# Kernel optimization log

Measured on AMD Instinct MI355X. Metric: run time of the kernel, lower is better.

Reference implementation:

```python
import jax, jax.numpy as jnp
import numpy as np

C = 32
KSHAPE = (C, C, 3, 3)  # (C_out, C_in, kH, kW)
BN_EPS = 1e-5


def _binary_act(x):
    # forward: sign(x); backward: identity clipped to |x|<1 (STE)
    xc = jnp.clip(x, -1.0, 1.0)
    return jax.lax.stop_gradient(jnp.sign(x) - xc) + xc


def _binarize_weight(w_flat, shape):
    w = w_flat.reshape(shape)
    scale = jax.lax.stop_gradient(jnp.mean(jnp.abs(w)))  # global scalar scale, detached
    wc = jnp.clip(w, -1.0, 1.0)
    # forward: scale*sign(w); backward flows through clamp(w,-1,1)
    return jax.lax.stop_gradient(scale * jnp.sign(w) - wc) + wc


def _bi_conv_bn(x, w_flat, gamma, beta, stride):
    xb = _binary_act(x)
    w = _binarize_weight(w_flat, KSHAPE)
    y = jax.lax.conv_general_dilated(
        xb, w, window_strides=(stride, stride), padding=[(1, 1), (1, 1)],
        dimension_numbers=('NCHW', 'OIHW', 'NCHW'))
    # BatchNorm2d in training mode (batch stats, biased variance)
    m = jnp.mean(y, axis=(0, 2, 3), keepdims=True)
    v = jnp.mean((y - m) ** 2, axis=(0, 2, 3), keepdims=True)
    yhat = (y - m) * jax.lax.rsqrt(v + BN_EPS)
    return gamma.reshape(1, -1, 1, 1) * yhat + beta.reshape(1, -1, 1, 1)


def setup_inputs() -> dict:
    key = jax.random.key(0)
    k1, k2, k3 = jax.random.split(key, 3)
    return {
        'x': jax.random.normal(k1, (32, C, 160, 160), dtype=jnp.float32),
        'w1': jax.random.normal(k2, (C * C * 9, 1), dtype=jnp.float32) * 0.05,
        'gamma1': jnp.ones((C,), dtype=jnp.float32),
        'beta1': jnp.zeros((C,), dtype=jnp.float32),
        'w2': jax.random.normal(k3, (C * C * 9, 1), dtype=jnp.float32) * 0.05,
        'gamma2': jnp.ones((C,), dtype=jnp.float32),
        'beta2': jnp.zeros((C,), dtype=jnp.float32),
    }


def reference(x, w1, gamma1, beta1, w2, gamma2, beta2):
    # bireal residual block, stride=1 => skip_op is Identity
    inner = _bi_conv_bn(x, w1, gamma1, beta1, 1) + x
    out = _bi_conv_bn(inner, w2, gamma2, beta2, 1) + inner
    return out
```

## Files before the change

kernel.cpp:

```cpp
#include <hip/hip_runtime.h>
#include <stdint.h>

#define NIMG 32
#define CH 32
#define HH 160
#define WW 160
#define HWL (HH*WW)
#define PRS 164
#define PHH 162
#define PIMG (PHH*PRS)
#define NPIX (NIMG*HWL)
#define HALO_WORDS 968

#define OFF_P     0
#define OFF_P2    3400704
#define OFF_INNER (OFF_P2 + 3400704)
#define OFF_WP    (OFF_INNER + 52428800)
#define OFF_CORR  (OFF_WP + 2304)
#define OFF_SC    (OFF_CORR + 2304)
#define OFF_SB    (OFF_SC + 128)

struct StatLine {
  int s1; int pad0; unsigned long long s2; char pad[112];
};

#define AS1 __attribute__((address_space(1)))
#define AS3 __attribute__((address_space(3)))
__device__ __forceinline__ void dma16(const void* g, void* l) {
  __builtin_amdgcn_global_load_lds((const AS1 void*)g, (AS3 void*)l, 16, 0, 0);
}

__device__ __forceinline__ unsigned short f2bf(float f) {
  unsigned u = __float_as_uint(f);
  u += 0x7fffu + ((u >> 16) & 1u);
  return (unsigned short)(u >> 16);
}
__device__ __forceinline__ float bf2f(unsigned short u) {
  return __uint_as_float((uint32_t)u << 16);
}

__device__ __forceinline__ void conv4(const uint32_t r[3][6], const uint32_t* wsh,
                                      int co, int& a0, int& a1, int& a2, int& a3)
{
  a0 = a1 = a2 = a3 = 0;
  #pragma unroll
  for (int dy = 0; dy < 3; ++dy) {
    #pragma unroll
    for (int dx = 0; dx < 3; ++dx) {
      uint32_t wvv = wsh[co * 9 + dy * 3 + dx];
      a0 += __popc(r[dy][0 + dx] ^ wvv);
      a1 += __popc(r[dy][1 + dx] ^ wvv);
      a2 += __popc(r[dy][2 + dx] ^ wvv);
      a3 += __popc(r[dy][3 + dx] ^ wvv);
    }
  }
}

__global__ __launch_bounds__(256) void pack_prep(const float* __restrict__ x,
    const float* __restrict__ w1, const float* __restrict__ w2,
    uint32_t* __restrict__ P, uint32_t* __restrict__ P2, uint32_t* __restrict__ WP,
    int* __restrict__ CORR, float* __restrict__ SC, StatLine* __restrict__ SB)
{
  __shared__ float lds[8192];
  const int tid = threadIdx.x;
  const int b = blockIdx.x;

  if (b >= 3200) {
    if (b == 3442) {
      int* z = (int*)SB;
      for (int i = tid; i < 2048; i += 256) z[i] = 0;
      float* red = lds;
      uint32_t* wpl = (uint32_t*)(lds + 256);
      for (int cv = 0; cv < 2; ++cv) {
        const float* w = cv ? w2 : w1;
        float s = 0.f;
        #pragma unroll
        for (int j = 0; j < 9; ++j) {
          float4 v = *reinterpret_cast<const float4*>(w + (j * 256 + tid) * 4);
          s += fabsf(v.x) + fabsf(v.y) + fabsf(v.z) + fabsf(v.w);
        }
        red[tid] = s;
        __syncthreads();
        for (int st = 128; st > 0; st >>= 1) {
          if (tid < st) red[tid] += red[tid + st];
          __syncthreads();
        }
        if (tid == 0) SC[cv] = red[0] / 9216.0f;
        for (int i = tid; i < 288; i += 256) {
          int co = i / 9, t = i - co * 9;
          uint32_t bw = 0;
          for (int ci = 0; ci < 32; ++ci)
            bw |= (w[(co * 32 + ci) * 9 + t] > 0.0f) ? (1u << ci) : 0u;
          WP[cv * 288 + i] = bw;
          wpl[i] = bw;
        }
        __syncthreads();
        for (int i = tid; i < 288; i += 256) {
          int cls = i / 32, co = i - cls * 32;
          int hc = cls / 3, wc = cls - hc * 3;
          int corr = 0;
          for (int t = 0; t < 9; ++t) {
            int dy = t / 3 - 1, dx = t % 3 - 1;
            bool inval = (hc == 0 && dy == -1) || (hc == 2 && dy == 1) ||
                         (wc == 0 && dx == -1) || (wc == 2 && dx == 1);
            if (inval) corr += 32 - 2 * __popc(wpl[co * 9 + t]);
          }
          CORR[cv * 288 + cls * 32 + co] = corr;
        }
        __syncthreads();
      }
    } else {
      int k = (b - 3200) * 256 + tid;
      uint32_t* buf = (k < 32 * HALO_WORDS) ? P : P2;
      int j = k % (32 * HALO_WORDS);
      int img = j / HALO_WORDS;
      int r = j - img * HALO_WORDS;
      int pr, pc;
      if (r < 164)      { pr = 0;   pc = r; }
      else if (r < 328) { pr = 161; pc = r - 164; }
      else {
        int k2 = r - 328;
        pr = 1 + (k2 >> 2);
        int q = k2 & 3;
        pc = (q == 0) ? 0 : (160 + q);
      }
      buf[img * PIMG + pr * PRS + pc] = 0;
    }
    return;
  }

  int n = b / 100;
  int p0 = (b - n * 100) * 256;
  const float* xb = x + (size_t)n * CH * HWL + p0;
  #pragma unroll
  for (int it = 0; it < 8; ++it) {
    int c = it * 4 + (tid >> 6);
    const float* g = xb + (size_t)c * HWL + (tid & 63) * 4;
    dma16(g, lds + c * 256);
  }
  __syncthreads();

  uint32_t bits = 0;
  #pragma unroll
  for (int c = 0; c < 32; ++c) {
    if (lds[c * 256 + tid] > 0.f) bits |= 1u << c;
  }
  int px = p0 + tid;
  int h = px / WW, w = px - h * WW;
  P[n * PIMG + (h + 1) * PRS + (w + 1)] = bits;
}

__global__ __launch_bounds__(256) void conv_stats(const uint32_t* __restrict__ P,
    const uint32_t* __restrict__ WP, const int* __restrict__ CORR,
    StatLine* __restrict__ sb)
{
  __shared__ uint32_t wsh[288];
  __shared__ int csh[288];
  __shared__ int ls1[32], ls2[32];
  const int tid = threadIdx.x;
  for (int i = tid; i < 288; i += 256) { wsh[i] = WP[i]; csh[i] = CORR[i]; }
  if (tid < 32) { ls1[tid] = 0; ls2[tid] = 0; }
  __syncthreads();

  int g = blockIdx.x * 256 + tid;
  int w4 = g % 40;
  int t1 = g / 40;
  int h = t1 % 160;
  int n = t1 / 160;

  const uint32_t* base = P + n * PIMG + h * PRS + w4 * 4;
  uint32_t r[3][6];
  #pragma unroll
  for (int dy = 0; dy < 3; ++dy) {
    uint4 a = *reinterpret_cast<const uint4*>(base + dy * PRS);
    uint2 bw = *reinterpret_cast<const uint2*>(base + dy * PRS + 4);
    r[dy][0] = a.x; r[dy][1] = a.y; r[dy][2] = a.z; r[dy][3] = a.w;
    r[dy][4] = bw.x; r[dy][5] = bw.y;
  }

  int rowc = (h == 0) ? 0 : ((h == 159) ? 6 : 3);
  int cls0  = rowc + ((w4 == 0) ? 0 : 1);
  int cls12 = rowc + 1;
  int cls3  = rowc + ((w4 == 39) ? 2 : 1);
  int lane = tid & 63;

  #pragma unroll
  for (int co = 0; co < 32; ++co) {
    int a0, a1, a2, a3;
    conv4(r, wsh, co, a0, a1, a2, a3);
    int d0 = 288 - 2 * a0 - csh[cls0 * 32 + co];
    int d1 = 288 - 2 * a1 - csh[cls12 * 32 + co];
    int d2 = 288 - 2 * a2 - csh[cls12 * 32 + co];
    int d3 = 288 - 2 * a3 - csh[cls3 * 32 + co];
    int ds = d0 + d1 + d2 + d3;
    int sq = d0 * d0 + d1 * d1 + d2 * d2 + d3 * d3;
    #pragma unroll
    for (int off = 32; off > 0; off >>= 1) {
      ds += __shfl_down(ds, off);
      sq += __shfl_down(sq, off);
    }
    if (lane == 0) { atomicAdd(&ls1[co], ds); atomicAdd(&ls2[co], sq); }
  }
  __syncthreads();
  if (tid < 32) {
    atomicAdd(&sb[tid].s1, ls1[tid]);
    atomicAdd(&sb[tid].s2, (unsigned long long)(long long)ls2[tid]);
  }
}

__global__ __launch_bounds__(256, 2) void conv_bn1(const uint32_t* __restrict__ P,
    const uint32_t* __restrict__ WP, const int* __restrict__ CORR,
    const float* __restrict__ x, const float* __restrict__ SCp,
    const StatLine* __restrict__ sb, const float* __restrict__ gamma,
    const float* __restrict__ beta, unsigned short* __restrict__ INNER,
    uint32_t* __restrict__ P2)
{
  __shared__ uint32_t wsh[288];
  __shared__ int csh[288];
  __shared__ float Ash[32], Bsh[32];
  const int tid = threadIdx.x;
  for (int i = tid; i < 288; i += 256) { wsh[i] = WP[i]; csh[i] = CORR[i]; }
  if (tid < 32) {
    double sc = (double)SCp[0];
    double m  = sc * (double)sb[tid].s1 / (double)NPIX;
    double ms = sc * sc * (double)(long long)sb[tid].s2 / (double)NPIX;
    float inv = (float)(1.0 / sqrt(ms - m * m + 1e-5));
    float gm = gamma[tid];
    Ash[tid] = gm * inv * (float)sc;
    Bsh[tid] = beta[tid] - gm * inv * (float)m;
  }
  __syncthreads();

  int g = blockIdx.x * 256 + tid;
  int w4 = g % 40;
  int t1 = g / 40;
  int h = t1 % 160;
  int n = t1 / 160;

  const uint32_t* base = P + n * PIMG + h * PRS + w4 * 4;
  uint32_t r[3][6];
  #pragma unroll
  for (int dy = 0; dy < 3; ++dy) {
    uint4 a = *reinterpret_cast<const uint4*>(base + dy * PRS);
    uint2 bw = *reinterpret_cast<const uint2*>(base + dy * PRS + 4);
    r[dy][0] = a.x; r[dy][1] = a.y; r[dy][2] = a.z; r[dy][3] = a.w;
    r[dy][4] = bw.x; r[dy][5] = bw.y;
  }
  int rowc = (h == 0) ? 0 : ((h == 159) ? 6 : 3);
  int cls0  = rowc + ((w4 == 0) ? 0 : 1);
  int cls12 = rowc + 1;
  int cls3  = rowc + ((w4 == 39) ? 2 : 1);

  int i = h * WW + w4 * 4;
  size_t pbase = (size_t)n * CH * HWL + i;

  float4 xv[32];
  #pragma unroll
  for (int j = 0; j < 32; ++j)
    xv[j] = *reinterpret_cast<const float4*>(x + pbase + (size_t)j * HWL);

  uint32_t bb0 = 0, bb1 = 0, bb2 = 0, bb3 = 0;
  #pragma unroll
  for (int co = 0; co < 32; ++co) {
    int a0, a1, a2, a3;
    conv4(r, wsh, co, a0, a1, a2, a3);
    int d0 = 288 - 2 * a0 - csh[cls0 * 32 + co];
    int d1 = 288 - 2 * a1 - csh[cls12 * 32 + co];
    int d2 = 288 - 2 * a2 - csh[cls12 * 32 + co];
    int d3 = 288 - 2 * a3 - csh[cls3 * 32 + co];
    float A = Ash[co], Bv = Bsh[co];
    float v0 = fmaf(A, (float)d0, Bv) + xv[co].x;
    float v1 = fmaf(A, (float)d1, Bv) + xv[co].y;
    float v2 = fmaf(A, (float)d2, Bv) + xv[co].z;
    float v3 = fmaf(A, (float)d3, Bv) + xv[co].w;
    ushort4 o; o.x = f2bf(v0); o.y = f2bf(v1); o.z = f2bf(v2); o.w = f2bf(v3);
    *reinterpret_cast<ushort4*>(INNER + pbase + (size_t)co * HWL) = o;
    uint32_t m = 1u << co;
    if (v0 > 0.f) bb0 |= m;
    if (v1 > 0.f) bb1 |= m;
    if (v2 > 0.f) bb2 |= m;
    if (v3 > 0.f) bb3 |= m;
  }
  uint32_t* pw = P2 + n * PIMG + (h + 1) * PRS + (w4 * 4 + 1);
  pw[0] = bb0; pw[1] = bb1; pw[2] = bb2; pw[3] = bb3;
}

__global__ __launch_bounds__(256, 2) void conv_bn2(const uint32_t* __restrict__ P2,
    const uint32_t* __restrict__ WP, const int* __restrict__ CORR,
    const unsigned short* __restrict__ INNER, const float* __restrict__ SCp,
    const StatLine* __restrict__ sb, const float* __restrict__ gamma,
    const float* __restrict__ beta, float* __restrict__ out)
{
  __shared__ uint32_t wsh[288];
  __shared__ int csh[288];
  __shared__ float Ash[32], Bsh[32];
  const int tid = threadIdx.x;
  for (int i = tid; i < 288; i += 256) { wsh[i] = WP[i]; csh[i] = CORR[i]; }
  if (tid < 32) {
    double sc = (double)SCp[0];
    double m  = sc * (double)sb[tid].s1 / (double)NPIX;
    double ms = sc * sc * (double)(long long)sb[tid].s2 / (double)NPIX;
    float inv = (float)(1.0 / sqrt(ms - m * m + 1e-5));
    float gm = gamma[tid];
    Ash[tid] = gm * inv * (float)sc;
    Bsh[tid] = beta[tid] - gm * inv * (float)m;
  }
  __syncthreads();

  int g = blockIdx.x * 256 + tid;
  int w4 = g % 40;
  int t1 = g / 40;
  int h = t1 % 160;
  int n = t1 / 160;

  const uint32_t* base = P2 + n * PIMG + h * PRS + w4 * 4;
  uint32_t r[3][6];
  #pragma unroll
  for (int dy = 0; dy < 3; ++dy) {
    uint4 a = *reinterpret_cast<const uint4*>(base + dy * PRS);
    uint2 bw = *reinterpret_cast<const uint2*>(base + dy * PRS + 4);
    r[dy][0] = a.x; r[dy][1] = a.y; r[dy][2] = a.z; r[dy][3] = a.w;
    r[dy][4] = bw.x; r[dy][5] = bw.y;
  }
  int rowc = (h == 0) ? 0 : ((h == 159) ? 6 : 3);
  int cls0  = rowc + ((w4 == 0) ? 0 : 1);
  int cls12 = rowc + 1;
  int cls3  = rowc + ((w4 == 39) ? 2 : 1);

  int i = h * WW + w4 * 4;
  size_t pbase = (size_t)n * CH * HWL + i;

  ushort4 iv[32];
  #pragma unroll
  for (int j = 0; j < 32; ++j)
    iv[j] = *reinterpret_cast<const ushort4*>(INNER + pbase + (size_t)j * HWL);

  #pragma unroll
  for (int co = 0; co < 32; ++co) {
    int a0, a1, a2, a3;
    conv4(r, wsh, co, a0, a1, a2, a3);
    int d0 = 288 - 2 * a0 - csh[cls0 * 32 + co];
    int d1 = 288 - 2 * a1 - csh[cls12 * 32 + co];
    int d2 = 288 - 2 * a2 - csh[cls12 * 32 + co];
    int d3 = 288 - 2 * a3 - csh[cls3 * 32 + co];
    float A = Ash[co], Bv = Bsh[co];
    float4 o;
    o.x = fmaf(A, (float)d0, Bv) + bf2f(iv[co].x);
    o.y = fmaf(A, (float)d1, Bv) + bf2f(iv[co].y);
    o.z = fmaf(A, (float)d2, Bv) + bf2f(iv[co].z);
    o.w = fmaf(A, (float)d3, Bv) + bf2f(iv[co].w);
    *reinterpret_cast<float4*>(out + pbase + (size_t)co * HWL) = o;
  }
}

extern "C" void kernel_launch(void* const* d_in, const int* in_sizes, int n_in,
                              void* d_out, int out_size, void* d_ws, size_t ws_size,
                              hipStream_t stream)
{
  (void)in_sizes; (void)n_in; (void)out_size; (void)ws_size;
  const float* x  = (const float*)d_in[0];
  const float* w1 = (const float*)d_in[1];
  const float* g1 = (const float*)d_in[2];
  const float* b1 = (const float*)d_in[3];
  const float* w2 = (const float*)d_in[4];
  const float* g2 = (const float*)d_in[5];
  const float* b2 = (const float*)d_in[6];
  float* out = (float*)d_out;
  char* ws = (char*)d_ws;

  uint32_t*       P     = (uint32_t*)(ws + OFF_P);
  uint32_t*       P2    = (uint32_t*)(ws + OFF_P2);
  unsigned short* INNER = (unsigned short*)(ws + OFF_INNER);
  uint32_t*       WP    = (uint32_t*)(ws + OFF_WP);
  int*            CORR  = (int*)(ws + OFF_CORR);
  float*          SC    = (float*)(ws + OFF_SC);
  StatLine*       SB    = (StatLine*)(ws + OFF_SB);

  pack_prep<<<3443, 256, 0, stream>>>(x, w1, w2, P, P2, WP, CORR, SC, SB);
  conv_stats<<<800, 256, 0, stream>>>(P, WP, CORR, SB);
  conv_bn1<<<800, 256, 0, stream>>>(P, WP, CORR, x, SC, SB, g1, b1, INNER, P2);
  conv_stats<<<800, 256, 0, stream>>>(P2, WP + 288, CORR + 288, SB + 32);
  conv_bn2<<<800, 256, 0, stream>>>(P2, WP + 288, CORR + 288, INNER, SC + 1, SB + 32, g2, b2, out);
}
```

Measured before the change: 176.1 us.

## Stage x via LDS DMA in conv_bn1 and store inner as pixel-major bf16

conv_bn1 now processes one pixel per thread over 3200 blocks. Its x tile is staged into LDS with global_load_lds, overlapped with the binary-row loads and the BN-affine setup. The bf16 intermediate is stored pixel-major (32 channels contiguous per pixel, written as four uint4 per pixel) instead of channel-planar, so conv_bn2 reads 64 contiguous bytes per pixel as uint4 vectors. The change is meant to replace the many strided per-channel global loads and stores with contiguous vector accesses. In exchange, conv_bn1 loses the 4-pixel popcount reuse and the occupancy hint, and conv_bn2 needs extra register unpacking.

After: 201.5 us. +14.4%, slower.

```diff
diff --git a/kernel.cpp b/kernel.cpp
--- a/kernel.cpp
+++ b/kernel.cpp
@@ -14,8 +14,8 @@
 
 #define OFF_P     0
 #define OFF_P2    3400704
-#define OFF_INNER (OFF_P2 + 3400704)
-#define OFF_WP    (OFF_INNER + 52428800)
+#define OFF_IT    (OFF_P2 + 3400704)
+#define OFF_WP    (OFF_IT + 52428800)
 #define OFF_CORR  (OFF_WP + 2304)
 #define OFF_SC    (OFF_CORR + 2304)
 #define OFF_SB    (OFF_SC + 128)
@@ -54,6 +54,18 @@
       a3 += __popc(r[dy][3 + dx] ^ wvv);
     }
   }
+}
+
+__device__ __forceinline__ void bn_affine(const float* SCp, const StatLine* sb,
+    const float* gamma, const float* beta, int c, float& A, float& B)
+{
+  double sc = (double)SCp[0];
+  double m  = sc * (double)sb[c].s1 / (double)NPIX;
+  double ms = sc * sc * (double)(long long)sb[c].s2 / (double)NPIX;
+  float inv = (float)(1.0 / sqrt(ms - m * m + 1e-5));
+  float gm = gamma[c];
+  A = gm * inv * (float)sc;
+  B = beta[c] - gm * inv * (float)m;
 }
 
 __global__ __launch_bounds__(256) void pack_prep(const float* __restrict__ x,
@@ -135,8 +147,7 @@
   #pragma unroll
   for (int it = 0; it < 8; ++it) {
     int c = it * 4 + (tid >> 6);
-    const float* g = xb + (size_t)c * HWL + (tid & 63) * 4;
-    dma16(g, lds + c * 256);
+    dma16(xb + (size_t)c * HWL + (tid & 63) * 4, lds + c * 256);
   }
   __syncthreads();
 
@@ -208,27 +219,86 @@
   }
 }
 
-__global__ __launch_bounds__(256, 2) void conv_bn1(const uint32_t* __restrict__ P,
+__global__ __launch_bounds__(256) void conv_bn1(const uint32_t* __restrict__ P,
     const uint32_t* __restrict__ WP, const int* __restrict__ CORR,
     const float* __restrict__ x, const float* __restrict__ SCp,
     const StatLine* __restrict__ sb, const float* __restrict__ gamma,
-    const float* __restrict__ beta, unsigned short* __restrict__ INNER,
+    const float* __restrict__ beta, unsigned short* __restrict__ IT,
     uint32_t* __restrict__ P2)
+{
+  __shared__ float xs[8192];
+  __shared__ uint32_t wsh[288];
+  __shared__ int csh[288];
+  __shared__ float Ash[32], Bsh[32];
+  const int tid = threadIdx.x;
+  const int b = blockIdx.x;
+  int n = b / 100;
+  int p0 = (b - n * 100) * 256;
+  const float* xb = x + (size_t)n * CH * HWL + p0;
+
+  #pragma unroll
+  for (int it = 0; it < 8; ++it) {
+    int c = it * 4 + (tid >> 6);
+    dma16(xb + (size_t)c * HWL + (tid & 63) * 4, xs + c * 256);
+  }
+
+  for (int i = tid; i < 288; i += 256) { wsh[i] = WP[i]; csh[i] = CORR[i]; }
+  if (tid < 32) bn_affine(SCp, sb, gamma, beta, tid, Ash[tid], Bsh[tid]);
+
+  int px = p0 + tid;
+  int h = px / WW, w = px - h * WW;
+  const uint32_t* bp = P + n * PIMG + h * PRS + w;
+  uint32_t r9[3][3];
+  #pragma unroll
+  for (int dy = 0; dy < 3; ++dy) {
+    r9[dy][0] = bp[dy * PRS + 0];
+    r9[dy][1] = bp[dy * PRS + 1];
+    r9[dy][2] = bp[dy * PRS + 2];
+  }
+  int hc = (h == 0) ? 0 : ((h == 159) ? 2 : 1);
+  int wc = (w == 0) ? 0 : ((w == 159) ? 2 : 1);
+  int cls = hc * 3 + wc;
+
+  __syncthreads();
+
+  uint32_t bits = 0;
+  uint32_t ow[16];
+  #pragma unroll
+  for (int co = 0; co < 32; ++co) {
+    int a = 0;
+    #pragma unroll
+    for (int dy = 0; dy < 3; ++dy) {
+      #pragma unroll
+      for (int dx = 0; dx < 3; ++dx)
+        a += __popc(r9[dy][dx] ^ wsh[co * 9 + dy * 3 + dx]);
+    }
+    int d = 288 - 2 * a - csh[cls * 32 + co];
+    float v = fmaf(Ash[co], (float)d, Bsh[co]) + xs[co * 256 + tid];
+    if (v > 0.f) bits |= 1u << co;
+    uint32_t bf = (uint32_t)f2bf(v);
+    if ((co & 1) == 0) ow[co >> 1] = bf;
+    else               ow[co >> 1] |= bf << 16;
+  }
+  P2[n * PIMG + (h + 1) * PRS + (w + 1)] = bits;
+  uint4* ip = (uint4*)(IT + (size_t)(n * HWL + px) * 32);
+  ip[0] = make_uint4(ow[0], ow[1], ow[2], ow[3]);
+  ip[1] = make_uint4(ow[4], ow[5], ow[6], ow[7]);
+  ip[2] = make_uint4(ow[8], ow[9], ow[10], ow[11]);
+  ip[3] = make_uint4(ow[12], ow[13], ow[14], ow[15]);
+}
+
+__global__ __launch_bounds__(256, 2) void conv_bn2(const uint32_t* __restrict__ P2,
+    const uint32_t* __restrict__ WP, const int* __restrict__ CORR,
+    const unsigned short* __restrict__ IT, const float* __restrict__ SCp,
+    const StatLine* __restrict__ sb, const float* __restrict__ gamma,
+    const float* __restrict__ beta, float* __restrict__ out)
 {
   __shared__ uint32_t wsh[288];
   __shared__ int csh[288];
   __shared__ float Ash[32], Bsh[32];
   const int tid = threadIdx.x;
   for (int i = tid; i < 288; i += 256) { wsh[i] = WP[i]; csh[i] = CORR[i]; }
-  if (tid < 32) {
-    double sc = (double)SCp[0];
-    double m  = sc * (double)sb[tid].s1 / (double)NPIX;
-    double ms = sc * sc * (double)(long long)sb[tid].s2 / (double)NPIX;
-    float inv = (float)(1.0 / sqrt(ms - m * m + 1e-5));
-    float gm = gamma[tid];
-    Ash[tid] = gm * inv * (float)sc;
-    Bsh[tid] = beta[tid] - gm * inv * (float)m;
-  }
+  if (tid < 32) bn_affine(SCp, sb, gamma, beta, tid, Ash[tid], Bsh[tid]);
   __syncthreads();
 
   int g = blockIdx.x * 256 + tid;
@@ -237,7 +307,7 @@
   int h = t1 % 160;
   int n = t1 / 160;
 
-  const uint32_t* base = P + n * PIMG + h * PRS + w4 * 4;
+  const uint32_t* base = P2 + n * PIMG + h * PRS + w4 * 4;
   uint32_t r[3][6];
   #pragma unroll
   for (int dy = 0; dy < 3; ++dy) {
@@ -254,101 +324,40 @@
   int i = h * WW + w4 * 4;
   size_t pbase = (size_t)n * CH * HWL + i;
 
-  float4 xv[32];
-  #pragma unroll
-  for (int j = 0; j < 32; ++j)
-    xv[j] = *reinterpret_cast<const float4*>(x + pbase + (size_t)j * HWL);
-
-  uint32_t bb0 = 0, bb1 = 0, bb2 = 0, bb3 = 0;
+  uint4 tt[16];
+  const uint4* ip = (const uint4*)(IT + (size_t)(n * HWL + i) * 32);
+  #pragma unroll
+  for (int q = 0; q < 16; ++q) tt[q] = ip[q];
+
   #pragma unroll
   for (int co = 0; co < 32; ++co) {
-    int a0, a1, a2, a3;
-    conv4(r, wsh, co, a0, a1, a2, a3);
-    int d0 = 288 - 2 * a0 - csh[cls0 * 32 + co];
-    int d1 = 288 - 2 * a1 - csh[cls12 * 32 + co];
-    int d2 = 288 - 2 * a2 - csh[cls12 * 32 + co];
-    int d3 = 288 - 2 * a3 - csh[cls3 * 32 + co];
+    int e0, e1, e2, e3;
+    conv4(r, wsh, co, e0, e1, e2, e3);
+    int f0 = 288 - 2 * e0 - csh[cls0 * 32 + co];
+    int f1 = 288 - 2 * e1 - csh[cls12 * 32 + co];
+    int f2 = 288 - 2 * e2 - csh[cls12 * 32 + co];
+    int f3 = 288 - 2 * e3 - csh[cls3 * 32 + co];
     float A = Ash[co], Bv = Bsh[co];
-    float v0 = fmaf(A, (float)d0, Bv) + xv[co].x;
-    float v1 = fmaf(A, (float)d1, Bv) + xv[co].y;
-    float v2 = fmaf(A, (float)d2, Bv) + xv[co].z;
-    float v3 = fmaf(A, (float)d3, Bv) + xv[co].w;
-    ushort4 o; o.x = f2bf(v0); o.y = f2bf(v1); o.z = f2bf(v2); o.w = f2bf(v3);
-    *reinterpret_cast<ushort4*>(INNER + pbase + (size_t)co * HWL) = o;
-    uint32_t m = 1u << co;
-    if (v0 > 0.f) bb0 |= m;
-    if (v1 > 0.f) bb1 |= m;
-    if (v2 > 0.f) bb2 |= m;
-    if (v3 > 0.f) bb3 |= m;
-  }
-  uint32_t* pw = P2 + n * PIMG + (h + 1) * PRS + (w4 * 4 + 1);
-  pw[0] = bb0; pw[1] = bb1; pw[2] = bb2; pw[3] = bb3;
-}
-
-__global__ __launch_bounds__(256, 2) void conv_bn2(const uint32_t* __restrict__ P2,
-    const uint32_t* __restrict__ WP, const int* __restrict__ CORR,
-    const unsigned short* __restrict__ INNER, const float* __restrict__ SCp,
-    const StatLine* __restrict__ sb, const float* __restrict__ gamma,
-    const float* __restrict__ beta, float* __restrict__ out)
-{
-  __shared__ uint32_t wsh[288];
-  __shared__ int csh[288];
-  __shared__ float Ash[32], Bsh[32];
-  const int tid = threadIdx.x;
-  for (int i = tid; i < 288; i += 256) { wsh[i] = WP[i]; csh[i] = CORR[i]; }
-  if (tid < 32) {
-    double sc = (double)SCp[0];
-    double m  = sc * (double)sb[tid].s1 / (double)NPIX;
-    double ms = sc * sc * (double)(long long)sb[tid].s2 / (double)NPIX;
-    float inv = (float)(1.0 / sqrt(ms - m * m + 1e-5));
-    float gm = gamma[tid];
-    Ash[tid] = gm * inv * (float)sc;
-    Bsh[tid] = beta[tid] - gm * inv * (float)m;
-  }
-  __syncthreads();
-
-  int g = blockIdx.x * 256 + tid;
-  int w4 = g % 40;
-  int t1 = g / 40;
-  int h = t1 % 160;
-  int n = t1 / 160;
-
-  const uint32_t* base = P2 + n * PIMG + h * PRS + w4 * 4;
-  uint32_t r[3][6];
-  #pragma unroll
-  for (int dy = 0; dy < 3; ++dy) {
-    uint4 a = *reinterpret_cast<const uint4*>(base + dy * PRS);
-    uint2 bw = *reinterpret_cast<const uint2*>(base + dy * PRS + 4);
-    r[dy][0] = a.x; r[dy][1] = a.y; r[dy][2] = a.z; r[dy][3] = a.w;
-    r[dy][4] = bw.x; r[dy][5] = bw.y;
-  }
-  int rowc = (h == 0) ? 0 : ((h == 159) ? 6 : 3);
-  int cls0  = rowc + ((w4 == 0) ? 0 : 1);
-  int cls12 = rowc + 1;
-  int cls3  = rowc + ((w4 == 39) ? 2 : 1);
-
-  int i = h * WW + w4 * 4;
-  size_t pbase = (size_t)n * CH * HWL + i;
-
-  ushort4 iv[32];
-  #pragma unroll
-  for (int j = 0; j < 32; ++j)
-    iv[j] = *reinterpret_cast<const ushort4*>(INNER + pbase + (size_t)j * HWL);
-
-  #pragma unroll
-  for (int co = 0; co < 32; ++co) {
-    int a0, a1, a2, a3;
-    conv4(r, wsh, co, a0, a1, a2, a3);
-    int d0 = 288 - 2 * a0 - csh[cls0 * 32 + co];
-    int d1 = 288 - 2 * a1 - csh[cls12 * 32 + co];
-    int d2 = 288 - 2 * a2 - csh[cls12 * 32 + co];
-    int d3 = 288 - 2 * a3 - csh[cls3 * 32 + co];
-    float A = Ash[co], Bv = Bsh[co];
+    const int qw = co >> 3;
+    const int ws = (co >> 1) & 3;
+    const int hf = co & 1;
+    uint32_t u0 = (ws == 0) ? tt[0 * 4 + qw].x : (ws == 1) ? tt[0 * 4 + qw].y
+                : (ws == 2) ? tt[0 * 4 + qw].z : tt[0 * 4 + qw].w;
+    uint32_t u1 = (ws == 0) ? tt[1 * 4 + qw].x : (ws == 1) ? tt[1 * 4 + qw].y
+                : (ws == 2) ? tt[1 * 4 + qw].z : tt[1 * 4 + qw].w;
+    uint32_t u2 = (ws == 0) ? tt[2 * 4 + qw].x : (ws == 1) ? tt[2 * 4 + qw].y
+                : (ws == 2) ? tt[2 * 4 + qw].z : tt[2 * 4 + qw].w;
+    uint32_t u3 = (ws == 0) ? tt[3 * 4 + qw].x : (ws == 1) ? tt[3 * 4 + qw].y
+                : (ws == 2) ? tt[3 * 4 + qw].z : tt[3 * 4 + qw].w;
+    float i0 = bf2f((unsigned short)(hf ? (u0 >> 16) : (u0 & 0xffff)));
+    float i1 = bf2f((unsigned short)(hf ? (u1 >> 16) : (u1 & 0xffff)));
+    float i2 = bf2f((unsigned short)(hf ? (u2 >> 16) : (u2 & 0xffff)));
+    float i3 = bf2f((unsigned short)(hf ? (u3 >> 16) : (u3 & 0xffff)));
     float4 o;
-    o.x = fmaf(A, (float)d0, Bv) + bf2f(iv[co].x);
-    o.y = fmaf(A, (float)d1, Bv) + bf2f(iv[co].y);
-    o.z = fmaf(A, (float)d2, Bv) + bf2f(iv[co].z);
-    o.w = fmaf(A, (float)d3, Bv) + bf2f(iv[co].w);
+    o.x = fmaf(A, (float)f0, Bv) + i0;
+    o.y = fmaf(A, (float)f1, Bv) + i1;
+    o.z = fmaf(A, (float)f2, Bv) + i2;
+    o.w = fmaf(A, (float)f3, Bv) + i3;
     *reinterpret_cast<float4*>(out + pbase + (size_t)co * HWL) = o;
   }
 }
@@ -368,17 +377,17 @@
   float* out = (float*)d_out;
   char* ws = (char*)d_ws;
 
-  uint32_t*       P     = (uint32_t*)(ws + OFF_P);
-  uint32_t*       P2    = (uint32_t*)(ws + OFF_P2);
-  unsigned short* INNER = (unsigned short*)(ws + OFF_INNER);
-  uint32_t*       WP    = (uint32_t*)(ws + OFF_WP);
-  int*            CORR  = (int*)(ws + OFF_CORR);
-  float*          SC    = (float*)(ws + OFF_SC);
-  StatLine*       SB    = (StatLine*)(ws + OFF_SB);
+  uint32_t*       P    = (uint32_t*)(ws + OFF_P);
+  uint32_t*       P2   = (uint32_t*)(ws + OFF_P2);
+  unsigned short* IT   = (unsigned short*)(ws + OFF_IT);
+  uint32_t*       WP   = (uint32_t*)(ws + OFF_WP);
+  int*            CORR = (int*)(ws + OFF_CORR);
+  float*          SC   = (float*)(ws + OFF_SC);
+  StatLine*       SB   = (StatLine*)(ws + OFF_SB);
 
   pack_prep<<<3443, 256, 0, stream>>>(x, w1, w2, P, P2, WP, CORR, SC, SB);
   conv_stats<<<800, 256, 0, stream>>>(P, WP, CORR, SB);
-  conv_bn1<<<800, 256, 0, stream>>>(P, WP, CORR, x, SC, SB, g1, b1, INNER, P2);
+  conv_bn1<<<3200, 256, 0, stream>>>(P, WP, CORR, x, SC, SB, g1, b1, IT, P2);
   conv_stats<<<800, 256, 0, stream>>>(P2, WP + 288, CORR + 288, SB + 32);
-  conv_bn2<<<800, 256, 0, stream>>>(P2, WP + 288, CORR + 288, INNER, SC + 1, SB + 32, g2, b2, out);
-}
+  conv_bn2<<<800, 256, 0, stream>>>(P2, WP + 288, CORR + 288, IT, SC + 1, SB + 32, g2, b2, out);
+}
```
